# Performance work log

Hardware: AMD Instinct MI355X
Metric: run time of the kernel (lower is better)

The kernel has to match this reference:

```python
import jax, jax.numpy as jnp
import numpy as np

B, L, D = 256, 512, 64          # batch, seq_length, input_size
HE, HD, S, NC = 1024, 1024, 24, 2  # hidden_enc, hidden_dec, steps, num_classes
ALPHA, BETA = 0.3, 0.5
COLS = jnp.array([1, 2])        # ES_Normalize columns


def _gru(x, h0, Wih, Whh, bih, bhh):
    """torch nn.GRU (1 layer, batch_first). x: [B,T,Din], h0: [B,H]."""
    def step(h, xt):
        gi = xt @ Wih.T + bih              # [B, 3H]
        gh = h @ Whh.T + bhh               # [B, 3H]
        ir, iz, inn = jnp.split(gi, 3, axis=-1)
        hr, hz, hn = jnp.split(gh, 3, axis=-1)
        r = jax.nn.sigmoid(ir + hr)
        z = jax.nn.sigmoid(iz + hz)
        n = jnp.tanh(inn + r * hn)
        h_new = (1.0 - z) * n + z * h
        return h_new, h_new
    hT, hs = jax.lax.scan(step, h0, jnp.swapaxes(x, 0, 1))
    return jnp.swapaxes(hs, 0, 1), hT      # [B,T,H], [B,H]


def _es_normalize(x, a):
    # torch version does x.clone().detach() -> gradient is cut here
    x = jax.lax.stop_gradient(x)
    def step(prev, xt):
        o = (1.0 - a) * xt + a * prev      # out[i] = (1-a)*x[i] + a*out[i-1]
        return o, o
    _, outs = jax.lax.scan(step, x[:, 0, :], jnp.swapaxes(x[:, 1:, :], 0, 1))
    out = jnp.concatenate([x[:, :1, :], jnp.swapaxes(outs, 0, 1)], axis=1)
    st = out[:, -1:, COLS]                 # pre_step=0 -> last step, columns [1,2]
    return out, st


def setup_inputs() -> dict:
    key = jax.random.key(0)
    ks = jax.random.split(key, 14)
    def u(k, shape, fan):
        b = 1.0 / np.sqrt(fan)
        return jax.random.uniform(k, shape, jnp.float32, -b, b)
    return {
        "x": jax.random.normal(ks[0], (B, L, D), jnp.float32),
        "enc_Wih": u(ks[1], (3 * HE, D), HE),
        "enc_Whh": u(ks[2], (3 * HE, HE), HE),
        "enc_bih": u(ks[3], (3 * HE,), HE),
        "enc_bhh": u(ks[4], (3 * HE,), HE),
        "dec_Wih": u(ks[5], (3 * HD, HE), HD),
        "dec_Whh": u(ks[6], (3 * HD, HD), HD),
        "dec_bih": u(ks[7], (3 * HD,), HD),
        "dec_bhh": u(ks[8], (3 * HD,), HD),
        "fci_W": u(ks[9], (HD, HE), HE),
        "fci_b": u(ks[10], (HD,), HE),
        "fc_W": u(ks[11], (NC, HD), HD),
        "fc_b": u(ks[12], (NC,), HD),
    }


def reference(x, enc_Wih, enc_Whh, enc_bih, enc_bhh,
              dec_Wih, dec_Whh, dec_bih, dec_bhh,
              fci_W, fci_b, fc_W, fc_b):
    b = x.shape[0]
    x1, st11 = _es_normalize(x, ALPHA)
    x2, st12 = _es_normalize(x1, BETA)
    h0 = jnp.zeros((b, HE), x.dtype)
    _, hT = _gru(x2, h0, enc_Wih, enc_Whh, enc_bih, enc_bhh)   # [B, HE]
    h0d = hT @ fci_W.T + fci_b                                  # fc_init_hidden_status
    # repeat + view: decoder input is encoder final state tiled over steps
    dec_in = jnp.broadcast_to(hT[:, None, :], (b, S, HE))
    dec_out, _ = _gru(dec_in, h0d, dec_Wih, dec_Whh, dec_bih, dec_bhh)  # [B,S,HD]
    out = dec_out @ fc_W.T + fc_b                               # [B, S, NC]
    # ES_DeNormalize: st is a snapshot (torch.cat copies), so the per-step loop
    # x[:,i]=(x[:,i]-a*st[:,i])/(1-a) is fully vectorizable.
    st2 = jnp.concatenate([st12, out[:, :S - 1, :]], axis=1)
    out = (out - BETA * st2) / (1.0 - BETA)
    st1 = jnp.concatenate([st11, out[:, :S - 1, :]], axis=1)
    out = (out - ALPHA * st1) / (1.0 - ALPHA)
    return out.reshape(b, S * NC)
```

## Files before the change

### kernel.cpp

```cpp
#include <hip/hip_runtime.h>

typedef _Float16 half8  __attribute__((ext_vector_type(8)));
typedef _Float16 half4v __attribute__((ext_vector_type(4)));
typedef float    float4v __attribute__((ext_vector_type(4)));

#define MFMA16(a, b, c) __builtin_amdgcn_mfma_f32_16x16x32_f16((a), (b), (c), 0, 0, 0)

constexpr int BB = 256;
constexpr int LL = 512;
constexpr int DD = 64;
constexpr int HH = 1024;
constexpr int SS = 24;

constexpr size_t OFF_X2    = 0;
constexpr size_t SZ_X2     = (size_t)BB * LL * DD * 2;
constexpr size_t OFF_HBUF  = OFF_X2 + SZ_X2;
constexpr size_t SZ_HBUF   = (size_t)2 * BB * HH * 2;
constexpr size_t OFF_OUTP  = OFF_HBUF + SZ_HBUF;
constexpr size_t SZ_OUTP   = (size_t)BB * SS * 2 * 4;
constexpr size_t OFF_BAR   = OFF_OUTP + SZ_OUTP;
constexpr size_t SZ_BAR    = 32 * 4;
constexpr size_t OFF_EFLAG = OFF_BAR + SZ_BAR;
constexpr size_t SZ_EFLAG  = (size_t)8 * 32 * 16 * 4;
constexpr size_t OFF_ST11  = OFF_EFLAG + SZ_EFLAG;
constexpr size_t OFF_ST12  = OFF_ST11 + 2048;
constexpr size_t OFF_FLAG  = OFF_ST12 + 2048;

__device__ __forceinline__ void agstore_u64(void* p, unsigned long long v) {
  __hip_atomic_store((unsigned long long*)p, v, __ATOMIC_RELAXED, __HIP_MEMORY_SCOPE_AGENT);
}
__device__ __forceinline__ void agstore_u32(void* p, unsigned v) {
  __hip_atomic_store((unsigned*)p, v, __ATOMIC_RELAXED, __HIP_MEMORY_SCOPE_AGENT);
}
__device__ __forceinline__ unsigned agload_u32(const unsigned* p) {
  return __hip_atomic_load(p, __ATOMIC_RELAXED, __HIP_MEMORY_SCOPE_AGENT);
}
__device__ __forceinline__ half8 agload_h8(const _Float16* p) {
  const unsigned long long* q = (const unsigned long long*)p;
  union { unsigned long long u[2]; half8 h; } cv;
  cv.u[0] = __hip_atomic_load(q,     __ATOMIC_RELAXED, __HIP_MEMORY_SCOPE_AGENT);
  cv.u[1] = __hip_atomic_load(q + 1, __ATOMIC_RELAXED, __HIP_MEMORY_SCOPE_AGENT);
  return cv.h;
}
__device__ __forceinline__ void agstore_h4(void* p, half4v h) {
  union { half4v h; unsigned long long u; } cv; cv.h = h;
  agstore_u64(p, cv.u);
}

template <int M, int N>
__device__ __forceinline__ void zero_acc(float4v (&a)[M][N]) {
  #pragma unroll
  for (int m = 0; m < M; ++m) {
    #pragma unroll
    for (int n = 0; n < N; ++n) {
      #pragma unroll
      for (int r = 0; r < 4; ++r) a[m][n][r] = 0.f;
    }
  }
}

__device__ __forceinline__ half8 ld_w8_f16(const float* p) {
  float4 f0 = *(const float4*)(p);
  float4 f1 = *(const float4*)(p + 4);
  half8 h;
  h[0] = (_Float16)f0.x; h[1] = (_Float16)f0.y; h[2] = (_Float16)f0.z; h[3] = (_Float16)f0.w;
  h[4] = (_Float16)f1.x; h[5] = (_Float16)f1.y; h[6] = (_Float16)f1.z; h[7] = (_Float16)f1.w;
  return h;
}

__device__ __forceinline__ void load_W_frags(const float* __restrict__ W, int s, int w,
                                             int lane, half8 BW[6][8]) {
  const int l15 = lane & 15, lq = lane >> 4;
  #pragma unroll
  for (int n = 0; n < 6; ++n) {
    const int row = (n >> 1) * 1024 + s * 32 + (n & 1) * 16 + l15;
    const float* rp = W + (size_t)row * HH + (w << 8) + (lq << 3);
    #pragma unroll
    for (int ks = 0; ks < 8; ++ks) BW[n][ks] = ld_w8_f16(rp + ks * 32);
  }
}

__device__ __forceinline__ void bar_arrive(unsigned* ef, int lb, unsigned ep1) {
  __syncthreads();
  if (threadIdx.x == 0) agstore_u32(&ef[lb * 16], ep1);
}
__device__ __forceinline__ void bar_wait(unsigned* ef, unsigned ep) {
  if (threadIdx.x < 32) {
    while (agload_u32(&ef[threadIdx.x * 16]) < ep)
      __builtin_amdgcn_s_sleep(1);
  }
  __syncthreads();
}

__device__ __forceinline__ void wait_my8(unsigned* ef, int w8, unsigned ep, int lane) {
  for (;;) {
    unsigned f = 0xFFFFFFFFu;
    if (lane < 8) f = agload_u32(&ef[(w8 + lane) * 16]);
    unsigned long long m = __ballot(f >= ep);
    if (m == ~0ull) break;
    __builtin_amdgcn_s_sleep(1);
  }
}

__device__ __forceinline__ void flag_barrier(unsigned* flags, int blk, int tid, unsigned val) {
  __syncthreads();
  if (tid == 0) agstore_u32(&flags[blk], val);
  while (agload_u32(&flags[tid]) != val)
    __builtin_amdgcn_s_sleep(2);
  __syncthreads();
}

#define PS(rw, cl) (P[(rw)*97 + (cl)] + P[3104 + (rw)*97 + (cl)] + \
                    P[6208 + (rw)*97 + (cl)] + P[9312 + (rw)*97 + (cl)])

__global__ __launch_bounds__(256, 1) void ts_fused(
    const float* __restrict__ x,
    const float* __restrict__ eWih, const float* __restrict__ eWhh,
    const float* __restrict__ ebih, const float* __restrict__ ebhh,
    const float* __restrict__ dWih, const float* __restrict__ dWhh,
    const float* __restrict__ dbih, const float* __restrict__ dbhh,
    const float* __restrict__ fciW, const float* __restrict__ fcib,
    const float* __restrict__ fcW,  const float* __restrict__ fcb,
    float* __restrict__ out, char* __restrict__ ws) {
  __shared__ float P[4 * 32 * 97];
  __shared__ float Q[32 * 97];

  _Float16* x2     = (_Float16*)(ws + OFF_X2);
  _Float16* hbuf   = (_Float16*)(ws + OFF_HBUF);
  float* outp      = (float*)(ws + OFF_OUTP);
  unsigned* bar    = (unsigned*)(ws + OFF_BAR);
  unsigned* eflags = (unsigned*)(ws + OFF_EFLAG);
  float* st11      = (float*)(ws + OFF_ST11);
  float* st12      = (float*)(ws + OFF_ST12);
  unsigned* flags  = (unsigned*)(ws + OFF_FLAG);

  const int tid  = threadIdx.x;
  const int blk  = blockIdx.x;
  const int lane = tid & 63;
  const int w    = tid >> 6;
  const int w8   = w << 3;
  const int l15  = lane & 15;
  const int lq   = lane >> 4;
  const int g    = blk & 7;
  const int s    = blk >> 3;
  const int eb   = tid >> 3;
  const int jq   = tid & 7;
  const int colb = s * 32 + jq * 4;

  if (blk < 64) {
    if (tid < 64) {
      const int idx = blk * 64 + tid;
      const int b = idx >> 4, dq = idx & 15, d = dq * 4;
      const float* xp = x + (size_t)b * LL * DD + d;
      _Float16* x2p = x2 + (size_t)b * LL * DD + d;
      float v1[4] = {0.f, 0.f, 0.f, 0.f}, v2[4] = {0.f, 0.f, 0.f, 0.f};
      #pragma unroll 1
      for (int t0 = 0; t0 < LL; t0 += 8) {
        float4 xb[8];
        #pragma unroll
        for (int u = 0; u < 8; ++u)
          xb[u] = *(const float4*)(xp + (size_t)(t0 + u) * DD);
        #pragma unroll
        for (int u = 0; u < 8; ++u) {
          const int t = t0 + u;
          const float xe[4] = {xb[u].x, xb[u].y, xb[u].z, xb[u].w};
          half4v hv;
          #pragma unroll
          for (int e = 0; e < 4; ++e) {
            v1[e] = (t == 0) ? xe[e] : 0.7f * xe[e] + 0.3f * v1[e];
            v2[e] = (t == 0) ? v1[e] : 0.5f * v1[e] + 0.5f * v2[e];
            hv[e] = (_Float16)v2[e];
          }
          agstore_h4(x2p + (size_t)t * DD, hv);
        }
      }
      if (dq == 0) {
        union { float f[2]; unsigned long long u; } c1, c2;
        c1.f[0] = v1[1]; c1.f[1] = v1[2];
        c2.f[0] = v2[1]; c2.f[1] = v2[2];
        agstore_u64(&st11[b * 2], c1.u);
        agstore_u64(&st12[b * 2], c2.u);
      }
    }
  } else {
    unsigned long long* zr = (unsigned long long*)(ws + OFF_HBUF);
    const int NZ = (int)((SZ_HBUF + SZ_OUTP + SZ_BAR + SZ_EFLAG) / 8);
    for (int i = (blk - 64) * 256 + tid; i < NZ; i += 192 * 256) agstore_u64(&zr[i], 0ull);
  }

  flag_barrier(flags, blk, tid, 1u);

  unsigned* ef      = eflags + g * 32 * 16;
  unsigned* gridbar = bar;

  half8 BW[6][8];
  load_W_frags(eWhh, s, w, lane, BW);
  half8 BWi[6][2];
  if (w == 0) {
    #pragma unroll
    for (int n = 0; n < 6; ++n) {
      const int row = (n >> 1) * 1024 + s * 32 + (n & 1) * 16 + l15;
      const float* rp = eWih + (size_t)row * DD + (lq << 3);
      #pragma unroll
      for (int ks = 0; ks < 2; ++ks) BWi[n][ks] = ld_w8_f16(rp + ks * 32);
    }
  }
  float ebr[4], ebz[4], ebin[4], ebhn[4];
  #pragma unroll
  for (int e = 0; e < 4; ++e) {
    const int c = colb + e;
    ebr[e]  = ebih[c] + ebhh[c];
    ebz[e]  = ebih[1024 + c] + ebhh[1024 + c];
    ebin[e] = ebih[2048 + c];
    ebhn[e] = ebhh[2048 + c];
  }
  float hold[4] = {0.f, 0.f, 0.f, 0.f};

  #pragma unroll 1
  for (int t = 0; t < LL; ++t) {
    const _Float16* hc = hbuf + (size_t)(t & 1) * BB * HH;
    _Float16* hnx = hbuf + (size_t)((t + 1) & 1) * BB * HH;

    float4v acc[2][6], accI[2][2];
    zero_acc(acc);
    zero_acc(accI);

    if (w == 0) {
      #pragma unroll
      for (int ks = 0; ks < 2; ++ks) {
        const _Float16* ap = x2 + (size_t)(g * 32 + l15) * (LL * DD) + (size_t)t * DD + ks * 32 + (lq << 3);
        half8 a0 = *(const half8*)ap;
        half8 a1 = *(const half8*)(ap + (size_t)16 * LL * DD);
        #pragma unroll
        for (int n = 0; n < 6; ++n) {
          if (n < 4) {
            acc[0][n] = MFMA16(a0, BWi[n][ks], acc[0][n]);
            acc[1][n] = MFMA16(a1, BWi[n][ks], acc[1][n]);
          } else {
            accI[0][n - 4] = MFMA16(a0, BWi[n][ks], accI[0][n - 4]);
            accI[1][n - 4] = MFMA16(a1, BWi[n][ks], accI[1][n - 4]);
          }
        }
      }
    }
    if (t > 0) wait_my8(ef, w8, (unsigned)t, lane);
    #pragma unroll
    for (int ks = 0; ks < 8; ++ks) {
      const _Float16* ap = hc + (size_t)(g * 32 + l15) * HH + (w << 8) + ks * 32 + (lq << 3);
      half8 a0 = agload_h8(ap);
      half8 a1 = agload_h8(ap + 16 * HH);
      #pragma unroll
      for (int n = 0; n < 6; ++n) {
        acc[0][n] = MFMA16(a0, BW[n][ks], acc[0][n]);
        acc[1][n] = MFMA16(a1, BW[n][ks], acc[1][n]);
      }
    }
    {
      float* Pw = P + w * 3104;
      #pragma unroll
      for (int m = 0; m < 2; ++m) {
        const int row0 = m * 16 + lq * 4;
        #pragma unroll
        for (int n = 0; n < 6; ++n) {
          const int col = (n >> 1) * 32 + (n & 1) * 16 + l15;
          #pragma unroll
          for (int r = 0; r < 4; ++r) Pw[(row0 + r) * 97 + col] = acc[m][n][r];
        }
      }
      if (w == 0) {
        #pragma unroll
        for (int m = 0; m < 2; ++m) {
          const int row0 = m * 16 + lq * 4;
          #pragma unroll
          for (int n2 = 0; n2 < 2; ++n2) {
            const int col = n2 * 16 + l15;
            #pragma unroll
            for (int r = 0; r < 4; ++r) Q[(row0 + r) * 97 + col] = accI[m][n2][r];
          }
        }
      }
    }
    __syncthreads();
    {
      half4v hh;
      #pragma unroll
      for (int e = 0; e < 4; ++e) {
        const int j = jq * 4 + e;
        const float Sr = PS(eb, j);
        const float Sz = PS(eb, 32 + j);
        const float Hn = PS(eb, 64 + j);
        const float rr = 1.f / (1.f + __expf(-(Sr + ebr[e])));
        const float zz = 1.f / (1.f + __expf(-(Sz + ebz[e])));
        const float aN = (Q[eb * 97 + j] + ebin[e]) + rr * (Hn + ebhn[e]);
        const float nn = 1.f - 2.f / (1.f + __expf(2.f * aN));
        const float hv = (1.f - zz) * nn + zz * hold[e];
        hold[e] = hv;
        hh[e] = (_Float16)hv;
      }
      agstore_h4(hnx + (size_t)(g * 32 + eb) * HH + s * 32 + jq * 4, hh);
    }
    bar_arrive(ef, s, (unsigned)(t + 1));
  }

  {
    wait_my8(ef, w8, (unsigned)LL, lane);
    const _Float16* hT = hbuf;
    float4v acc[2][6];
    zero_acc(acc);
    #pragma unroll 1
    for (int ks = 0; ks < 8; ++ks) {
      const _Float16* ap = hT + (size_t)(g * 32 + l15) * HH + (w << 8) + ks * 32 + (lq << 3);
      half8 a0 = agload_h8(ap);
      half8 a1 = agload_h8(ap + 16 * HH);
      #pragma unroll
      for (int n = 0; n < 6; ++n) {
        const int row = (n >> 1) * 1024 + s * 32 + (n & 1) * 16 + l15;
        half8 bf = ld_w8_f16(dWih + (size_t)row * HH + (w << 8) + ks * 32 + (lq << 3));
        acc[0][n] = MFMA16(a0, bf, acc[0][n]);
        acc[1][n] = MFMA16(a1, bf, acc[1][n]);
      }
    }
    {
      float* Pw = P + w * 3104;
      #pragma unroll
      for (int m = 0; m < 2; ++m) {
        const int row0 = m * 16 + lq * 4;
        #pragma unroll
        for (int n = 0; n < 6; ++n) {
          const int col = (n >> 1) * 32 + (n & 1) * 16 + l15;
          #pragma unroll
          for (int r = 0; r < 4; ++r) Pw[(row0 + r) * 97 + col] = acc[m][n][r];
        }
      }
    }
    __syncthreads();
    #pragma unroll
    for (int e = 0; e < 4; ++e) {
      const int j = jq * 4 + e;
      #pragma unroll
      for (int gate = 0; gate < 3; ++gate) {
        const int col = gate * 32 + j;
        Q[eb * 97 + col] = PS(eb, col) + dbih[gate * 1024 + s * 32 + j];
      }
    }
    __syncthreads();
    float4v acc2[2][2];
    zero_acc(acc2);
    #pragma unroll 1
    for (int ks = 0; ks < 8; ++ks) {
      const _Float16* ap = hT + (size_t)(g * 32 + l15) * HH + (w << 8) + ks * 32 + (lq << 3);
      half8 a0 = agload_h8(ap);
      half8 a1 = agload_h8(ap + 16 * HH);
      #pragma unroll
      for (int n2 = 0; n2 < 2; ++n2) {
        const int row = s * 32 + n2 * 16 + l15;
        half8 bf = ld_w8_f16(fciW + (size_t)row * HH + (w << 8) + ks * 32 + (lq << 3));
        acc2[0][n2] = MFMA16(a0, bf, acc2[0][n2]);
        acc2[1][n2] = MFMA16(a1, bf, acc2[1][n2]);
      }
    }
    {
      float* Pw = P + w * 3104;
      #pragma unroll
      for (int m = 0; m < 2; ++m) {
        const int row0 = m * 16 + lq * 4;
        #pragma unroll
        for (int n2 = 0; n2 < 2; ++n2) {
          const int col = n2 * 16 + l15;
          #pragma unroll
          for (int r = 0; r < 4; ++r) Pw[(row0 + r) * 97 + col] = acc2[m][n2][r];
        }
      }
    }
    __syncthreads();
    {
      half4v hh;
      #pragma unroll
      for (int e = 0; e < 4; ++e) {
        const int j = jq * 4 + e;
        const float v = PS(eb, j) + fcib[s * 32 + j];
        hold[e] = v;
        hh[e] = (_Float16)v;
      }
      agstore_h4(hbuf + (size_t)BB * HH + (size_t)(g * 32 + eb) * HH + s * 32 + jq * 4, hh);
    }
    bar_arrive(ef, s, (unsigned)(LL + 1));
  }

  load_W_frags(dWhh, s, w, lane, BW);
  float dbr_[4], dbz_[4], dbn_[4], fw0[4], fw1[4];
  #pragma unroll
  for (int e = 0; e < 4; ++e) {
    const int c = colb + e;
    dbr_[e] = dbhh[c];
    dbz_[e] = dbhh[1024 + c];
    dbn_[e] = dbhh[2048 + c];
    fw0[e] = fcW[c];
    fw1[e] = fcW[1024 + c];
  }
  #pragma unroll 1
  for (int t = 0; t < SS; ++t) {
    wait_my8(ef, w8, (unsigned)(LL + 1 + t), lane);
    const _Float16* hc = hbuf + (size_t)((t + 1) & 1) * BB * HH;
    _Float16* hnx = hbuf + (size_t)(t & 1) * BB * HH;
    float4v acc[2][6];
    zero_acc(acc);
    #pragma unroll
    for (int ks = 0; ks < 8; ++ks) {
      const _Float16* ap = hc + (size_t)(g * 32 + l15) * HH + (w << 8) + ks * 32 + (lq << 3);
      half8 a0 = agload_h8(ap);
      half8 a1 = agload_h8(ap + 16 * HH);
      #pragma unroll
      for (int n = 0; n < 6; ++n) {
        acc[0][n] = MFMA16(a0, BW[n][ks], acc[0][n]);
        acc[1][n] = MFMA16(a1, BW[n][ks], acc[1][n]);
      }
    }
    {
      float* Pw = P + w * 3104;
      #pragma unroll
      for (int m = 0; m < 2; ++m) {
        const int row0 = m * 16 + lq * 4;
        #pragma unroll
        for (int n = 0; n < 6; ++n) {
          const int col = (n >> 1) * 32 + (n & 1) * 16 + l15;
          #pragma unroll
          for (int r = 0; r < 4; ++r) Pw[(row0 + r) * 97 + col] = acc[m][n][r];
        }
      }
    }
    __syncthreads();
    {
      half4v hh;
      float p0 = 0.f, p1 = 0.f;
      #pragma unroll
      for (int e = 0; e < 4; ++e) {
        const int j = jq * 4 + e;
        const float rr = 1.f / (1.f + __expf(-(PS(eb, j) + Q[eb * 97 + j] + dbr_[e])));
        const float zz = 1.f / (1.f + __expf(-(PS(eb, 32 + j) + Q[eb * 97 + 32 + j] + dbz_[e])));
        const float aN = Q[eb * 97 + 64 + j] + rr * (PS(eb, 64 + j) + dbn_[e]);
        const float nn = 1.f - 2.f / (1.f + __expf(2.f * aN));
        const float hv = (1.f - zz) * nn + zz * hold[e];
        hold[e] = hv;
        hh[e] = (_Float16)hv;
        p0 += hv * fw0[e];
        p1 += hv * fw1[e];
      }
      agstore_h4(hnx + (size_t)(g * 32 + eb) * HH + s * 32 + jq * 4, hh);
      p0 += __shfl_xor(p0, 1); p0 += __shfl_xor(p0, 2); p0 += __shfl_xor(p0, 4);
      p1 += __shfl_xor(p1, 1); p1 += __shfl_xor(p1, 2); p1 += __shfl_xor(p1, 4);
      if (jq == 0) {
        atomicAdd(&outp[((g * 32 + eb) * SS + t) * 2 + 0], p0);
        atomicAdd(&outp[((g * 32 + eb) * SS + t) * 2 + 1], p1);
      }
    }
    bar_arrive(ef, s, (unsigned)(LL + 2 + t));
  }

  bar_wait(ef, (unsigned)(LL + 1 + SS));
  if (s == 0 && tid == 0) atomicAdd(gridbar, 1u);
  if (tid == 0) {
    while (agload_u32(gridbar) < 8u) __builtin_amdgcn_s_sleep(1);
  }
  __syncthreads();

  if (blk < 2) {
    const int t5 = blk * 256 + tid;
    const int b = t5 >> 1, c = t5 & 1;
    const float s2v = st12[b * 2 + c];
    const float s1v = st11[b * 2 + c];
    const float bias = fcb[c];
    float o0p = 0.f, o1p = 0.f;
    #pragma unroll 1
    for (int t = 0; t < SS; ++t) {
      const float o0 = outp[(b * SS + t) * 2 + c] + bias;
      const float o1 = 2.f * o0 - ((t == 0) ? s2v : o0p);
      const float o2 = (o1 - 0.3f * ((t == 0) ? s1v : o1p)) * (1.f / 0.7f);
      o0p = o0; o1p = o1;
      out[b * 48 + t * 2 + c] = o2;
    }
  }

  if (tid == 0) agstore_u32(&flags[blk], 0u);
}

extern "C" void kernel_launch(void* const* d_in, const int* in_sizes, int n_in,
                              void* d_out, int out_size, void* d_ws, size_t ws_size,
                              hipStream_t stream) {
  (void)in_sizes; (void)n_in; (void)out_size; (void)ws_size;
  const float* x    = (const float*)d_in[0];
  const float* eWih = (const float*)d_in[1];
  const float* eWhh = (const float*)d_in[2];
  const float* ebih = (const float*)d_in[3];
  const float* ebhh = (const float*)d_in[4];
  const float* dWih = (const float*)d_in[5];
  const float* dWhh = (const float*)d_in[6];
  const float* dbih = (const float*)d_in[7];
  const float* dbhh = (const float*)d_in[8];
  const float* fciW = (const float*)d_in[9];
  const float* fcib = (const float*)d_in[10];
  const float* fcW  = (const float*)d_in[11];
  const float* fcb  = (const float*)d_in[12];
  float* out = (float*)d_out;
  char* ws = (char*)d_ws;

  ts_fused<<<dim3(256), dim3(256), 0, stream>>>(
      x, eWih, eWhh, ebih, ebhh, dWih, dWhh, dbih, dbhh,
      fciW, fcib, fcW, fcb, out, ws);
}
```

Measured before the change: 3.634 ms.

## Double threads per block to split hidden-state K dimension across eight waves

```diff
diff --git a/kernel.cpp b/kernel.cpp
--- a/kernel.cpp
+++ b/kernel.cpp
@@ -46,6 +46,10 @@
   union { half4v h; unsigned long long u; } cv; cv.h = h;
   agstore_u64(p, cv.u);
 }
+__device__ __forceinline__ void agstore_h2(void* p, _Float16 h0, _Float16 h1) {
+  union { _Float16 h[2]; unsigned u; } cv; cv.h[0] = h0; cv.h[1] = h1;
+  agstore_u32(p, cv.u);
+}
 
 template <int M, int N>
 __device__ __forceinline__ void zero_acc(float4v (&a)[M][N]) {
@@ -69,14 +73,14 @@
 }
 
 __device__ __forceinline__ void load_W_frags(const float* __restrict__ W, int s, int w,
-                                             int lane, half8 BW[6][8]) {
+                                             int lane, half8 BW[6][4]) {
   const int l15 = lane & 15, lq = lane >> 4;
   #pragma unroll
   for (int n = 0; n < 6; ++n) {
     const int row = (n >> 1) * 1024 + s * 32 + (n & 1) * 16 + l15;
-    const float* rp = W + (size_t)row * HH + (w << 8) + (lq << 3);
-    #pragma unroll
-    for (int ks = 0; ks < 8; ++ks) BW[n][ks] = ld_w8_f16(rp + ks * 32);
+    const float* rp = W + (size_t)row * HH + (w << 7) + (lq << 3);
+    #pragma unroll
+    for (int ks = 0; ks < 4; ++ks) BW[n][ks] = ld_w8_f16(rp + ks * 32);
   }
 }
 
@@ -92,10 +96,10 @@
   __syncthreads();
 }
 
-__device__ __forceinline__ void wait_my8(unsigned* ef, int w8, unsigned ep, int lane) {
+__device__ __forceinline__ void wait_my4(unsigned* ef, int s0, unsigned ep, int lane) {
   for (;;) {
     unsigned f = 0xFFFFFFFFu;
-    if (lane < 8) f = agload_u32(&ef[(w8 + lane) * 16]);
+    if (lane < 4) f = agload_u32(&ef[(s0 + lane) * 16]);
     unsigned long long m = __ballot(f >= ep);
     if (m == ~0ull) break;
     __builtin_amdgcn_s_sleep(1);
@@ -105,15 +109,21 @@
 __device__ __forceinline__ void flag_barrier(unsigned* flags, int blk, int tid, unsigned val) {
   __syncthreads();
   if (tid == 0) agstore_u32(&flags[blk], val);
-  while (agload_u32(&flags[tid]) != val)
-    __builtin_amdgcn_s_sleep(2);
+  if (tid < 256) {
+    while (agload_u32(&flags[tid]) != val)
+      __builtin_amdgcn_s_sleep(2);
+  }
   __syncthreads();
 }
 
-#define PS(rw, cl) (P[(rw)*97 + (cl)] + P[3104 + (rw)*97 + (cl)] + \
-                    P[6208 + (rw)*97 + (cl)] + P[9312 + (rw)*97 + (cl)])
-
-__global__ __launch_bounds__(256, 1) void ts_fused(
+__device__ __forceinline__ float ps8(const float* P, int rw, int cl) {
+  float s = 0.f;
+  #pragma unroll
+  for (int u = 0; u < 8; ++u) s += P[u * 3104 + rw * 97 + cl];
+  return s;
+}
+
+__global__ __launch_bounds__(512, 2) void ts_fused(
     const float* __restrict__ x,
     const float* __restrict__ eWih, const float* __restrict__ eWhh,
     const float* __restrict__ ebih, const float* __restrict__ ebhh,
@@ -122,8 +132,8 @@
     const float* __restrict__ fciW, const float* __restrict__ fcib,
     const float* __restrict__ fcW,  const float* __restrict__ fcb,
     float* __restrict__ out, char* __restrict__ ws) {
-  __shared__ float P[4 * 32 * 97];
-  __shared__ float Q[32 * 97];
+  __shared__ float P[8 * 32 * 97];
+  __shared__ float Q[2 * 32 * 97];
 
   _Float16* x2     = (_Float16*)(ws + OFF_X2);
   _Float16* hbuf   = (_Float16*)(ws + OFF_HBUF);
@@ -138,14 +148,14 @@
   const int blk  = blockIdx.x;
   const int lane = tid & 63;
   const int w    = tid >> 6;
-  const int w8   = w << 3;
+  const int w4   = w << 2;
   const int l15  = lane & 15;
   const int lq   = lane >> 4;
   const int g    = blk & 7;
   const int s    = blk >> 3;
-  const int eb   = tid >> 3;
-  const int jq   = tid & 7;
-  const int colb = s * 32 + jq * 4;
+  const int eb   = tid >> 4;
+  const int jq   = tid & 15;
+  const int colb = s * 32 + jq * 2;
 
   if (blk < 64) {
     if (tid < 64) {
@@ -185,7 +195,7 @@
   } else {
     unsigned long long* zr = (unsigned long long*)(ws + OFF_HBUF);
     const int NZ = (int)((SZ_HBUF + SZ_OUTP + SZ_BAR + SZ_EFLAG) / 8);
-    for (int i = (blk - 64) * 256 + tid; i < NZ; i += 192 * 256) agstore_u64(&zr[i], 0ull);
+    for (int i = (blk - 64) * 512 + tid; i < NZ; i += 192 * 512) agstore_u64(&zr[i], 0ull);
   }
 
   flag_barrier(flags, blk, tid, 1u);
@@ -193,28 +203,26 @@
   unsigned* ef      = eflags + g * 32 * 16;
   unsigned* gridbar = bar;
 
-  half8 BW[6][8];
+  half8 BW[6][4];
   load_W_frags(eWhh, s, w, lane, BW);
-  half8 BWi[6][2];
-  if (w == 0) {
+  half8 BWi[6];
+  if (w < 2) {
     #pragma unroll
     for (int n = 0; n < 6; ++n) {
       const int row = (n >> 1) * 1024 + s * 32 + (n & 1) * 16 + l15;
-      const float* rp = eWih + (size_t)row * DD + (lq << 3);
-      #pragma unroll
-      for (int ks = 0; ks < 2; ++ks) BWi[n][ks] = ld_w8_f16(rp + ks * 32);
-    }
-  }
-  float ebr[4], ebz[4], ebin[4], ebhn[4];
+      BWi[n] = ld_w8_f16(eWih + (size_t)row * DD + (w << 5) + (lq << 3));
+    }
+  }
+  float ebr[2], ebz[2], ebin[2], ebhn[2];
   #pragma unroll
-  for (int e = 0; e < 4; ++e) {
+  for (int e = 0; e < 2; ++e) {
     const int c = colb + e;
     ebr[e]  = ebih[c] + ebhh[c];
     ebz[e]  = ebih[1024 + c] + ebhh[1024 + c];
     ebin[e] = ebih[2048 + c];
     ebhn[e] = ebhh[2048 + c];
   }
-  float hold[4] = {0.f, 0.f, 0.f, 0.f};
+  float hold[2] = {0.f, 0.f};
 
   #pragma unroll 1
   for (int t = 0; t < LL; ++t) {
@@ -225,34 +233,35 @@
     zero_acc(acc);
     zero_acc(accI);
 
-    if (w == 0) {
-      #pragma unroll
-      for (int ks = 0; ks < 2; ++ks) {
-        const _Float16* ap = x2 + (size_t)(g * 32 + l15) * (LL * DD) + (size_t)t * DD + ks * 32 + (lq << 3);
-        half8 a0 = *(const half8*)ap;
-        half8 a1 = *(const half8*)(ap + (size_t)16 * LL * DD);
-        #pragma unroll
-        for (int n = 0; n < 6; ++n) {
-          if (n < 4) {
-            acc[0][n] = MFMA16(a0, BWi[n][ks], acc[0][n]);
-            acc[1][n] = MFMA16(a1, BWi[n][ks], acc[1][n]);
-          } else {
-            accI[0][n - 4] = MFMA16(a0, BWi[n][ks], accI[0][n - 4]);
-            accI[1][n - 4] = MFMA16(a1, BWi[n][ks], accI[1][n - 4]);
-          }
-        }
-      }
-    }
-    if (t > 0) wait_my8(ef, w8, (unsigned)t, lane);
-    #pragma unroll
-    for (int ks = 0; ks < 8; ++ks) {
-      const _Float16* ap = hc + (size_t)(g * 32 + l15) * HH + (w << 8) + ks * 32 + (lq << 3);
-      half8 a0 = agload_h8(ap);
-      half8 a1 = agload_h8(ap + 16 * HH);
+    if (w < 2) {
+      const _Float16* ap = x2 + (size_t)(g * 32 + l15) * (LL * DD) + (size_t)t * DD + (w << 5) + (lq << 3);
+      half8 a0 = *(const half8*)ap;
+      half8 a1 = *(const half8*)(ap + (size_t)16 * LL * DD);
       #pragma unroll
       for (int n = 0; n < 6; ++n) {
-        acc[0][n] = MFMA16(a0, BW[n][ks], acc[0][n]);
-        acc[1][n] = MFMA16(a1, BW[n][ks], acc[1][n]);
+        if (n < 4) {
+          acc[0][n] = MFMA16(a0, BWi[n], acc[0][n]);
+          acc[1][n] = MFMA16(a1, BWi[n], acc[1][n]);
+        } else {
+          accI[0][n - 4] = MFMA16(a0, BWi[n], accI[0][n - 4]);
+          accI[1][n - 4] = MFMA16(a1, BWi[n], accI[1][n - 4]);
+        }
+      }
+    }
+    if (t > 0) wait_my4(ef, w4, (unsigned)t, lane);
+    half8 a0[4], a1[4];
+    #pragma unroll
+    for (int ks = 0; ks < 4; ++ks) {
+      const _Float16* ap = hc + (size_t)(g * 32 + l15) * HH + (w << 7) + ks * 32 + (lq << 3);
+      a0[ks] = agload_h8(ap);
+      a1[ks] = agload_h8(ap + 16 * HH);
+    }
+    #pragma unroll
+    for (int ks = 0; ks < 4; ++ks) {
+      #pragma unroll
+      for (int n = 0; n < 6; ++n) {
+        acc[0][n] = MFMA16(a0[ks], BW[n][ks], acc[0][n]);
+        acc[1][n] = MFMA16(a1[ks], BW[n][ks], acc[1][n]);
       }
     }
     {
@@ -267,7 +276,8 @@
           for (int r = 0; r < 4; ++r) Pw[(row0 + r) * 97 + col] = acc[m][n][r];
         }
       }
-      if (w == 0) {
+      if (w < 2) {
+        float* Qw = Q + w * 3104;
         #pragma unroll
         for (int m = 0; m < 2; ++m) {
           const int row0 = m * 16 + lq * 4;
@@ -275,47 +285,48 @@
           for (int n2 = 0; n2 < 2; ++n2) {
             const int col = n2 * 16 + l15;
             #pragma unroll
-            for (int r = 0; r < 4; ++r) Q[(row0 + r) * 97 + col] = accI[m][n2][r];
+            for (int r = 0; r < 4; ++r) Qw[(row0 + r) * 97 + col] = accI[m][n2][r];
           }
         }
       }
     }
     __syncthreads();
     {
-      half4v hh;
-      #pragma unroll
-      for (int e = 0; e < 4; ++e) {
-        const int j = jq * 4 + e;
-        const float Sr = PS(eb, j);
-        const float Sz = PS(eb, 32 + j);
-        const float Hn = PS(eb, 64 + j);
+      _Float16 hh[2];
+      #pragma unroll
+      for (int e = 0; e < 2; ++e) {
+        const int j = jq * 2 + e;
+        const float Sr = ps8(P, eb, j);
+        const float Sz = ps8(P, eb, 32 + j);
+        const float Hn = ps8(P, eb, 64 + j);
         const float rr = 1.f / (1.f + __expf(-(Sr + ebr[e])));
         const float zz = 1.f / (1.f + __expf(-(Sz + ebz[e])));
-        const float aN = (Q[eb * 97 + j] + ebin[e]) + rr * (Hn + ebhn[e]);
+        const float gin = Q[eb * 97 + j] + Q[3104 + eb * 97 + j];
+        const float aN = (gin + ebin[e]) + rr * (Hn + ebhn[e]);
         const float nn = 1.f - 2.f / (1.f + __expf(2.f * aN));
         const float hv = (1.f - zz) * nn + zz * hold[e];
         hold[e] = hv;
         hh[e] = (_Float16)hv;
       }
-      agstore_h4(hnx + (size_t)(g * 32 + eb) * HH + s * 32 + jq * 4, hh);
+      agstore_h2(hnx + (size_t)(g * 32 + eb) * HH + s * 32 + jq * 2, hh[0], hh[1]);
     }
     bar_arrive(ef, s, (unsigned)(t + 1));
   }
 
   {
-    wait_my8(ef, w8, (unsigned)LL, lane);
+    wait_my4(ef, w4, (unsigned)LL, lane);
     const _Float16* hT = hbuf;
     float4v acc[2][6];
     zero_acc(acc);
     #pragma unroll 1
-    for (int ks = 0; ks < 8; ++ks) {
-      const _Float16* ap = hT + (size_t)(g * 32 + l15) * HH + (w << 8) + ks * 32 + (lq << 3);
+    for (int ks = 0; ks < 4; ++ks) {
+      const _Float16* ap = hT + (size_t)(g * 32 + l15) * HH + (w << 7) + ks * 32 + (lq << 3);
       half8 a0 = agload_h8(ap);
       half8 a1 = agload_h8(ap + 16 * HH);
       #pragma unroll
       for (int n = 0; n < 6; ++n) {
         const int row = (n >> 1) * 1024 + s * 32 + (n & 1) * 16 + l15;
-        half8 bf = ld_w8_f16(dWih + (size_t)row * HH + (w << 8) + ks * 32 + (lq << 3));
+        half8 bf = ld_w8_f16(dWih + (size_t)row * HH + (w << 7) + ks * 32 + (lq << 3));
         acc[0][n] = MFMA16(a0, bf, acc[0][n]);
         acc[1][n] = MFMA16(a1, bf, acc[1][n]);
       }
@@ -335,26 +346,26 @@
     }
     __syncthreads();
     #pragma unroll
-    for (int e = 0; e < 4; ++e) {
-      const int j = jq * 4 + e;
+    for (int e = 0; e < 2; ++e) {
+      const int j = jq * 2 + e;
       #pragma unroll
       for (int gate = 0; gate < 3; ++gate) {
         const int col = gate * 32 + j;
-        Q[eb * 97 + col] = PS(eb, col) + dbih[gate * 1024 + s * 32 + j];
+        Q[eb * 97 + col] = ps8(P, eb, col) + dbih[gate * 1024 + s * 32 + j];
       }
     }
     __syncthreads();
     float4v acc2[2][2];
     zero_acc(acc2);
     #pragma unroll 1
-    for (int ks = 0; ks < 8; ++ks) {
-      const _Float16* ap = hT + (size_t)(g * 32 + l15) * HH + (w << 8) + ks * 32 + (lq << 3);
+    for (int ks = 0; ks < 4; ++ks) {
+      const _Float16* ap = hT + (size_t)(g * 32 + l15) * HH + (w << 7) + ks * 32 + (lq << 3);
       half8 a0 = agload_h8(ap);
       half8 a1 = agload_h8(ap + 16 * HH);
       #pragma unroll
       for (int n2 = 0; n2 < 2; ++n2) {
         const int row = s * 32 + n2 * 16 + l15;
-        half8 bf = ld_w8_f16(fciW + (size_t)row * HH + (w << 8) + ks * 32 + (lq << 3));
+        half8 bf = ld_w8_f16(fciW + (size_t)row * HH + (w << 7) + ks * 32 + (lq << 3));
         acc2[0][n2] = MFMA16(a0, bf, acc2[0][n2]);
         acc2[1][n2] = MFMA16(a1, bf, acc2[1][n2]);
       }
@@ -374,23 +385,23 @@
     }
     __syncthreads();
     {
-      half4v hh;
-      #pragma unroll
-      for (int e = 0; e < 4; ++e) {
-        const int j = jq * 4 + e;
-        const float v = PS(eb, j) + fcib[s * 32 + j];
+      _Float16 hh[2];
+      #pragma unroll
+      for (int e = 0; e < 2; ++e) {
+        const int j = jq * 2 + e;
+        const float v = ps8(P, eb, j) + fcib[s * 32 + j];
         hold[e] = v;
         hh[e] = (_Float16)v;
       }
-      agstore_h4(hbuf + (size_t)BB * HH + (size_t)(g * 32 + eb) * HH + s * 32 + jq * 4, hh);
+      agstore_h2(hbuf + (size_t)BB * HH + (size_t)(g * 32 + eb) * HH + s * 32 + jq * 2, hh[0], hh[1]);
     }
     bar_arrive(ef, s, (unsigned)(LL + 1));
   }
 
   load_W_frags(dWhh, s, w, lane, BW);
-  float dbr_[4], dbz_[4], dbn_[4], fw0[4], fw1[4];
+  float dbr_[2], dbz_[2], dbn_[2], fw0[2], fw1[2];
   #pragma unroll
-  for (int e = 0; e < 4; ++e) {
+  for (int e = 0; e < 2; ++e) {
     const int c = colb + e;
     dbr_[e] = dbhh[c];
     dbz_[e] = dbhh[1024 + c];
@@ -400,20 +411,24 @@
   }
   #pragma unroll 1
   for (int t = 0; t < SS; ++t) {
-    wait_my8(ef, w8, (unsigned)(LL + 1 + t), lane);
+    wait_my4(ef, w4, (unsigned)(LL + 1 + t), lane);
     const _Float16* hc = hbuf + (size_t)((t + 1) & 1) * BB * HH;
     _Float16* hnx = hbuf + (size_t)(t & 1) * BB * HH;
     float4v acc[2][6];
     zero_acc(acc);
-    #pragma unroll
-    for (int ks = 0; ks < 8; ++ks) {
-      const _Float16* ap = hc + (size_t)(g * 32 + l15) * HH + (w << 8) + ks * 32 + (lq << 3);
-      half8 a0 = agload_h8(ap);
-      half8 a1 = agload_h8(ap + 16 * HH);
+    half8 a0[4], a1[4];
+    #pragma unroll
+    for (int ks = 0; ks < 4; ++ks) {
+      const _Float16* ap = hc + (size_t)(g * 32 + l15) * HH + (w << 7) + ks * 32 + (lq << 3);
+      a0[ks] = agload_h8(ap);
+      a1[ks] = agload_h8(ap + 16 * HH);
+    }
+    #pragma unroll
+    for (int ks = 0; ks < 4; ++ks) {
       #pragma unroll
       for (int n = 0; n < 6; ++n) {
-        acc[0][n] = MFMA16(a0, BW[n][ks], acc[0][n]);
-        acc[1][n] = MFMA16(a1, BW[n][ks], acc[1][n]);
+        acc[0][n] = MFMA16(a0[ks], BW[n][ks], acc[0][n]);
+        acc[1][n] = MFMA16(a1[ks], BW[n][ks], acc[1][n]);
       }
     }
     {
@@ -431,14 +446,14 @@
     }
     __syncthreads();
     {
-      half4v hh;
+      _Float16 hh[2];
       float p0 = 0.f, p1 = 0.f;
       #pragma unroll
-      for (int e = 0; e < 4; ++e) {
-        const int j = jq * 4 + e;
-        const float rr = 1.f / (1.f + __expf(-(PS(eb, j) + Q[eb * 97 + j] + dbr_[e])));
-        const float zz = 1.f / (1.f + __expf(-(PS(eb, 32 + j) + Q[eb * 97 + 32 + j] + dbz_[e])));
-        const float aN = Q[eb * 97 + 64 + j] + rr * (PS(eb, 64 + j) + dbn_[e]);
+      for (int e = 0; e < 2; ++e) {
+        const int j = jq * 2 + e;
+        const float rr = 1.f / (1.f + __expf(-(ps8(P, eb, j) + Q[eb * 97 + j] + dbr_[e])));
+        const float zz = 1.f / (1.f + __expf(-(ps8(P, eb, 32 + j) + Q[eb * 97 + 32 + j] + dbz_[e])));
+        const float aN = Q[eb * 97 + 64 + j] + rr * (ps8(P, eb, 64 + j) + dbn_[e]);
         const float nn = 1.f - 2.f / (1.f + __expf(2.f * aN));
         const float hv = (1.f - zz) * nn + zz * hold[e];
         hold[e] = hv;
@@ -446,9 +461,9 @@
         p0 += hv * fw0[e];
         p1 += hv * fw1[e];
       }
-      agstore_h4(hnx + (size_t)(g * 32 + eb) * HH + s * 32 + jq * 4, hh);
-      p0 += __shfl_xor(p0, 1); p0 += __shfl_xor(p0, 2); p0 += __shfl_xor(p0, 4);
-      p1 += __shfl_xor(p1, 1); p1 += __shfl_xor(p1, 2); p1 += __shfl_xor(p1, 4);
+      agstore_h2(hnx + (size_t)(g * 32 + eb) * HH + s * 32 + jq * 2, hh[0], hh[1]);
+      p0 += __shfl_xor(p0, 1); p0 += __shfl_xor(p0, 2); p0 += __shfl_xor(p0, 4); p0 += __shfl_xor(p0, 8);
+      p1 += __shfl_xor(p1, 1); p1 += __shfl_xor(p1, 2); p1 += __shfl_xor(p1, 4); p1 += __shfl_xor(p1, 8);
       if (jq == 0) {
         atomicAdd(&outp[((g * 32 + eb) * SS + t) * 2 + 0], p0);
         atomicAdd(&outp[((g * 32 + eb) * SS + t) * 2 + 1], p1);
@@ -464,7 +479,7 @@
   }
   __syncthreads();
 
-  if (blk < 2) {
+  if (blk < 2 && tid < 256) {
     const int t5 = blk * 256 + tid;
     const int b = t5 >> 1, c = t5 & 1;
     const float s2v = st12[b * 2 + c];
@@ -504,7 +519,7 @@
   float* out = (float*)d_out;
   char* ws = (char*)d_ws;
 
-  ts_fused<<<dim3(256), dim3(256), 0, stream>>>(
+  ts_fused<<<dim3(256), dim3(512), 0, stream>>>(
       x, eWih, eWhh, ebih, ebhh, dWih, dWhh, dbih, dbhh,
       fciW, fcib, fcW, fcb, out, ws);
 }
```

Result: faster. 3.077 ms (-15.3%).
